# Kernel tuning notes

Measured on AMD Instinct MI355X. Metric: run time of the kernel, lower is better.

The kernel has to match this reference:

```python
import jax, jax.numpy as jnp
from jax import lax
import numpy as np

NINF = -1e10  # matches torch's -10000000000.0 masked fill


def setup_inputs() -> dict:
    B, T, Z, S1, X = 512, 1024, 8, 5, 2  # S1 = 2**stim_types + 1
    key = jax.random.key(0)
    k1, k2, k3, k4, k5, k6 = jax.random.split(key, 6)
    s = jax.random.randint(k1, (B, T), 0, S1)
    x = jax.random.randint(k2, (B, T), 0, X)
    mask = (jax.random.uniform(k3, (B, T)) > 0.1).astype(jnp.float32)
    # probability-simplex parameters (the torch model stores normalized pi/P/K)
    pi = jax.nn.softmax(jax.random.normal(k4, (Z,)))
    P = jax.nn.softmax(jax.random.normal(k5, (Z, X)), axis=-1)
    K = jax.nn.softmax(jax.random.normal(k6, (S1, Z, Z)), axis=-2)  # columns sum to 1 over 'to'
    return {"s": s, "x": x, "mask": mask, "pi": pi, "P": P, "K": K}


def reference(s, x, mask, pi, P, K):
    B, T = x.shape
    Z = pi.shape[0]
    logpi = jnp.log(pi)
    logP = jnp.log(P)            # (Z, X)
    logKb = jnp.log(K)[s]        # (B, T, Z, Z), [to, from]
    logPx = logP.T[x]            # (B, T, Z)

    # ---- forward pass: masked alpha recurrence ----
    def fstep(prev, inp):
        lK, lP, m = inp          # (B,Z,Z), (B,Z), (B,)
        new = (jax.nn.logsumexp(prev[:, None, :] + lK, axis=-1) + lP) * m[:, None] \
              + prev * (1.0 - m)[:, None]
        return new, new

    prev0 = jnp.broadcast_to(logpi[None, :], (B, Z))
    _, alphas = lax.scan(fstep, prev0,
                         (logKb.transpose(1, 0, 2, 3), logPx.transpose(1, 0, 2), mask.T))
    log_alpha = alphas.transpose(1, 0, 2)                 # (B, T, Z)
    loglik = jax.nn.logsumexp(log_alpha[:, -1, :], axis=-1)  # (B,)

    # ---- backward pass: masked beta recurrence (carries masked P/K 'next') ----
    def bstep(carry, inp):
        bn, lPn, lKn = carry
        lK_t, lP_t, m0, m1 = inp  # mask[t], mask[t+1]
        bt = jax.nn.logsumexp(lPn[:, :, None] + lKn + bn[:, :, None], axis=1) * m1[:, None] \
             + bn * (1.0 - m1)[:, None]
        lPn2 = lP_t * m0[:, None] + lPn * (1.0 - m0)[:, None]
        lKn2 = lK_t * m0[:, None, None] + lKn * (1.0 - m0)[:, None, None]
        return (bt, lPn2, lKn2), bt

    carry0 = (jnp.zeros((B, Z)), logPx[:, -1], logKb[:, -1])
    xs = (logKb[:, :-1].transpose(1, 0, 2, 3), logPx[:, :-1].transpose(1, 0, 2),
          mask[:, :-1].T, mask[:, 1:].T)
    _, betas = lax.scan(bstep, carry0, xs, reverse=True)
    log_beta = jnp.concatenate([betas.transpose(1, 0, 2), jnp.zeros((B, 1, Z))], axis=1)

    # ---- posteriors ----
    log_beta = log_beta - loglik[:, None, None]
    log_gamma = log_alpha + log_beta
    log_gamma = log_gamma - jax.nn.logsumexp(log_gamma, axis=-1, keepdims=True)
    log_xi = logKb[:, :-1] + log_alpha[:, :-1, :, None] + log_beta[:, 1:, None, :] \
             + logPx[:, 1:][:, :, None, :]
    log_xi = log_xi - jax.nn.logsumexp(log_xi.reshape(B, T - 1, -1), axis=-1)[:, :, None, None]
    log_gamma = jnp.where((mask == 0)[:, :, None], NINF, log_gamma)
    log_xi = jnp.where((mask[:, 1:] == 0)[:, :, None, None], NINF, log_xi)
    return log_gamma, log_xi, log_alpha, log_beta, loglik
```

## Files before the change

### kernel.cpp

```cpp
#include <hip/hip_runtime.h>

#define BB 512
#define TT 1024
#define GG 32
#define LL 32
#define NINF -10000000000.0f
#define SROW 65
#define NXROWS (BB * (TT - 1))
#define SCRATCH_ROW0 484375

template<int CTRL>
__device__ __forceinline__ float dppf(float x) {
    return __builtin_bit_cast(float, __builtin_amdgcn_update_dpp(
        0, __builtin_bit_cast(int, x), CTRL, 0xF, 0xF, true));
}
__device__ __forceinline__ float gsum8(float x) {
    x += dppf<0xB1>(x); x += dppf<0x4E>(x); x += dppf<0x141>(x); return x;
}
__device__ __forceinline__ float gmax8(float x) {
    x = fmaxf(x, dppf<0xB1>(x)); x = fmaxf(x, dppf<0x4E>(x)); x = fmaxf(x, dppf<0x141>(x)); return x;
}

#define GATHER8(A0, A1, A2, A3, A4, A5, A6, A7)      \
    const float A1 = dppf<0xB1>(A0);                 \
    const float A2 = dppf<0x4E>(A0);                 \
    const float A7 = dppf<0x141>(A0);                \
    const float A3 = dppf<0x4E>(A1);                 \
    const float A6 = dppf<0xB1>(A7);                 \
    const float A5 = dppf<0x4E>(A7);                 \
    const float A4 = dppf<0x4E>(A6);

#define FMASUM(ACC, K0, K1, A0,A1,A2,A3,A4,A5,A6,A7) \
    float ACC;                                       \
    {   float accA = K0.x * A0;                      \
        accA = fmaf(K0.y, A1, accA);                 \
        accA = fmaf(K0.z, A2, accA);                 \
        accA = fmaf(K0.w, A3, accA);                 \
        float accB = K1.x * A4;                      \
        accB = fmaf(K1.y, A5, accB);                 \
        accB = fmaf(K1.z, A6, accB);                 \
        ACC = accA + accB; }

__global__ __launch_bounds__(256) void segmat_kernel(
    const int* __restrict__ s, const int* __restrict__ x, const float* __restrict__ mask,
    const float* __restrict__ P, const float* __restrict__ K,
    float* __restrict__ FM, float* __restrict__ BM)
{
    __shared__ float kTab[5 * 68];
    __shared__ int   ctrlA[4][LL];
    const int tid = threadIdx.x;
    const int wv = tid >> 6, l = tid & 63;
    const int lo = l & 7, hi = l >> 3;
    const bool isF = blockIdx.x < 4096;
    const int task = (isF ? blockIdx.x : blockIdx.x - 4096) * 4 + wv;
    const int seq = task >> 5, seg = task & 31;
    const int sb = seq * TT;
    const int t0 = seg * LL;

    for (int e = tid; e < 340; e += 256) {
        const int ss = e / 68, idx = e - ss * 68;
        float v = 0.0f;
        if (idx < 64) {
            const int row = idx >> 3, r = idx & 7;
            v = isF ? K[ss*64 + row*8 + (row ^ r)]
                    : K[ss*64 + (row ^ r)*8 + row];
        }
        kTab[e] = v;
    }
    if (l < LL) {
        const int tt = t0 + l;
        ctrlA[wv][l] = s[sb+tt] | (x[sb+tt] << 3) | ((mask[sb+tt] != 0.0f) ? 16 : 0);
    }
    __syncthreads();

    const float pL0 = P[lo*2+0], pL1 = P[lo*2+1];
    const float* kbase = kTab + lo*8;
    float av = (lo == hi) ? 1.0f : 0.0f;
    float c = 0.0f;

    if (isF) {
#pragma unroll 4
        for (int u = 0; u < LL; ++u) {
            const int cw = __builtin_amdgcn_readfirstlane(ctrlA[wv][u]);
            if (cw & 16) {
                const float* kp = kbase + (cw & 7) * 68;
                const float4 k0 = *(const float4*)kp;
                const float4 k1 = *(const float4*)(kp + 4);
                const float a0 = av;
                GATHER8(a0, a1, a2, a3, a4, a5, a6, a7)
                FMASUM(acc, k0, k1, a0,a1,a2,a3,a4,a5,a6,a7)
                av = acc * ((cw & 8) ? pL1 : pL0);
            }
            if ((u & 3) == 3) {
                const float ms = gmax8(av);
                av *= __builtin_amdgcn_rcpf(ms);
                c += __logf(ms);
            }
        }
        FM[task*64 + l] = __logf(av) + c;
    } else {
        const int t1 = t0 + LL;
        int sxc = 0;
        for (int tt = t1; tt < TT; ++tt) {
            if (mask[sb + tt] != 0.0f) { sxc = s[sb+tt] | (x[sb+tt] << 3); break; }
        }
        int m1 = (t1 < TT && mask[sb + t1] != 0.0f) ? 16 : 0;
        sxc = __builtin_amdgcn_readfirstlane(sxc);
        m1  = __builtin_amdgcn_readfirstlane(m1);
#pragma unroll 4
        for (int u = LL - 1; u >= 0; --u) {
            const int cw = __builtin_amdgcn_readfirstlane(ctrlA[wv][u]);
            if (m1) {
                const float* kp = kbase + (sxc & 7) * 68;
                const float4 k0 = *(const float4*)kp;
                const float4 k1 = *(const float4*)(kp + 4);
                const float u0 = av * ((sxc & 8) ? pL1 : pL0);
                GATHER8(u0, u1, u2, u3, u4, u5, u6, u7)
                FMASUM(acc, k0, k1, u0,u1,u2,u3,u4,u5,u6,u7)
                av = acc;
            }
            sxc = (cw & 16) ? (cw & 15) : sxc;
            m1 = cw & 16;
            if ((u & 3) == 0) {
                const float ms = gmax8(av);
                av *= __builtin_amdgcn_rcpf(ms);
                c += __logf(ms);
            }
        }
        BM[task*64 + l] = __logf(av) + c;
    }
}

__global__ __launch_bounds__(256) void compose_kernel(
    const float* __restrict__ pi, const float* __restrict__ FM, const float* __restrict__ BM,
    float* __restrict__ SV, float* __restrict__ WV, float* __restrict__ loglik)
{
    const int tid = threadIdx.x;
    const int grp = blockIdx.x * 32 + (tid >> 3);
    const int i = tid & 7;
    if (grp < BB) {
        const int seq = grp;
        float v = __logf(pi[i]);
        for (int g = 0; g < GG; ++g) {
            SV[(seq*GG + g)*8 + i] = v;
            const float* M = FM + (size_t)(seq*GG + g) * 64;
            const float a0 = v;
            GATHER8(a0, a1, a2, a3, a4, a5, a6, a7)
            const float q0 = M[(i^0)*8 + i] + a0;
            const float q1 = M[(i^1)*8 + i] + a1;
            const float q2 = M[(i^2)*8 + i] + a2;
            const float q3 = M[(i^3)*8 + i] + a3;
            const float q4 = M[(i^4)*8 + i] + a4;
            const float q5 = M[(i^5)*8 + i] + a5;
            const float q6 = M[(i^6)*8 + i] + a6;
            const float q7 = M[(i^7)*8 + i] + a7;
            float m = fmaxf(q0, q1); m = fmaxf(m, q2); m = fmaxf(m, q3);
            m = fmaxf(m, q4); m = fmaxf(m, q5); m = fmaxf(m, q6); m = fmaxf(m, q7);
            float sum = __expf(q0-m) + __expf(q1-m) + __expf(q2-m) + __expf(q3-m)
                      + __expf(q4-m) + __expf(q5-m) + __expf(q6-m) + __expf(q7-m);
            v = m + __logf(sum);
        }
        const float gm = gmax8(v);
        const float ge = gsum8(__expf(v - gm));
        if (i == 0) loglik[seq] = gm + __logf(ge);
    } else {
        const int seq = grp - BB;
        float v = 0.0f;
        for (int g = GG - 1; g >= 0; --g) {
            WV[(seq*GG + g)*8 + i] = v;
            const float* M = BM + (size_t)(seq*GG + g) * 64;
            const float a0 = v;
            GATHER8(a0, a1, a2, a3, a4, a5, a6, a7)
            const float q0 = M[(i^0)*8 + i] + a0;
            const float q1 = M[(i^1)*8 + i] + a1;
            const float q2 = M[(i^2)*8 + i] + a2;
            const float q3 = M[(i^3)*8 + i] + a3;
            const float q4 = M[(i^4)*8 + i] + a4;
            const float q5 = M[(i^5)*8 + i] + a5;
            const float q6 = M[(i^6)*8 + i] + a6;
            const float q7 = M[(i^7)*8 + i] + a7;
            float m = fmaxf(q0, q1); m = fmaxf(m, q2); m = fmaxf(m, q3);
            m = fmaxf(m, q4); m = fmaxf(m, q5); m = fmaxf(m, q6); m = fmaxf(m, q7);
            float sum = __expf(q0-m) + __expf(q1-m) + __expf(q2-m) + __expf(q3-m)
                      + __expf(q4-m) + __expf(q5-m) + __expf(q6-m) + __expf(q7-m);
            v = m + __logf(sum);
        }
    }
}

__global__ __launch_bounds__(256) void fused_kernel(
    const int* __restrict__ s, const int* __restrict__ x, const float* __restrict__ mask,
    const float* __restrict__ P, const float* __restrict__ K,
    const float* __restrict__ SV, const float* __restrict__ WV,
    const float* __restrict__ loglik,
    float* __restrict__ alpha, float* __restrict__ beta,
    float* __restrict__ gamma, float* __restrict__ xi, int skipRow0)
{
    __shared__ float aLs[2 * 32 * SROW];
    __shared__ float bLs[2 * 33 * SROW];
    __shared__ int   ctrlL[2 * 33 * 8];
    __shared__ float kX[340], kTt[340];
    __shared__ float lK[320], lP[16];

    const int tid = threadIdx.x;
    const int wv = tid >> 6, l = tid & 63;
    const int lo = l & 7, g = l >> 3;
    const int sgp = blockIdx.x >> 4;
    const int pairIdx = blockIdx.x & 15;
    const int bfirst = sgp * 8;
    const int segi = wv >> 1;
    const bool isFwd = (wv & 1) == 0;
    const int seg = pairIdx * 2 + segi;
    const int t0 = seg * LL;
    const int seq = bfirst + g;
    const int sb = seq * TT;

    for (int e = tid; e < 340; e += 256) {
        const int ss = e / 68, idx = e - ss * 68;
        float vX = 0.0f, vT = 0.0f;
        if (idx < 64) {
            const int row = idx >> 3, r = idx & 7;
            vX = K[ss*64 + row*8 + (row ^ r)];
            vT = K[ss*64 + (row ^ r)*8 + row];
        }
        kX[e] = vX; kTt[e] = vT;
    }
    for (int e = tid; e < 320; e += 256) lK[e] = __logf(K[e]);
    if (tid < 16) lP[tid] = __logf(P[tid]);
    for (int e = tid; e < 528; e += 256) {
        const int si = e / 264, rem = e - si * 264;
        const int u = rem >> 3, gg = rem & 7;
        const int t = (pairIdx*2 + si)*LL + u;
        int cv = 0;
        if (t < TT) {
            const int a = (bfirst + gg)*TT + t;
            cv = s[a] | (x[a] << 3) | ((mask[a] != 0.0f) ? 16 : 0);
        }
        ctrlL[(si*33 + u)*8 + gg] = cv;
    }
    __syncthreads();

    const float pL0 = P[lo*2+0], pL1 = P[lo*2+1];

    if (isFwd) {
        const float sv0 = SV[(seq*GG + seg)*8 + lo];
        const float mx = gmax8(sv0);
        float av = __expf(sv0 - mx);
        float c = mx;
        size_t aoff = (size_t)(sb + t0)*8 + lo;
#pragma unroll 4
        for (int u = 0; u < LL; ++u) {
            const int cw = ctrlL[(segi*33 + u)*8 + g];
            const float* kp = kX + (cw & 7)*68 + lo*8;
            const float4 k0 = *(const float4*)kp;
            const float4 k1 = *(const float4*)(kp + 4);
            const float a0 = av;
            GATHER8(a0, a1, a2, a3, a4, a5, a6, a7)
            FMASUM(acc, k0, k1, a0,a1,a2,a3,a4,a5,a6,a7)
            const float nv = acc * ((cw & 8) ? pL1 : pL0);
            av = (cw & 16) ? nv : av;
            if ((u & 3) == 3) {
                const float ms = gmax8(av);
                av *= __builtin_amdgcn_rcpf(ms);
                c += __logf(ms);
            }
            const float la = __logf(av) + c;
            aLs[(segi*32 + u)*SROW + g*8 + lo] = la;
            __builtin_nontemporal_store(la, &alpha[aoff]);
            aoff += 8;
        }
    } else {
        const float w0 = WV[(seq*GG + seg)*8 + lo];
        const float llv = loglik[seq];
        const float mx = gmax8(w0);
        float bv = __expf(w0 - mx);
        float c = mx - llv;
        bLs[(segi*33 + 32)*SROW + g*8 + lo] = w0 - llv;
        const int t1 = t0 + LL;
        int m1 = ctrlL[(segi*33 + 32)*8 + g] & 16;
        int sxc = 0;
        {
            int tt = t1;
            int found = (t1 >= TT) ? 1 : 0;
            while (!__all(found)) {
                if (!found && tt < TT) {
                    if (mask[sb + tt] != 0.0f) { sxc = s[sb+tt] | (x[sb+tt] << 3); found = 1; }
                }
                if (tt >= TT - 1) found = 1;
                ++tt;
            }
        }
        size_t boff = (size_t)(sb + t1 - 1)*8 + lo;
#pragma unroll 4
        for (int u = LL - 1; u >= 0; --u) {
            const int cw = ctrlL[(segi*33 + u)*8 + g];
            const float* kp = kTt + (sxc & 7)*68 + lo*8;
            const float4 k0 = *(const float4*)kp;
            const float4 k1 = *(const float4*)(kp + 4);
            const float u0 = bv * ((sxc & 8) ? pL1 : pL0);
            GATHER8(u0, u1, u2, u3, u4, u5, u6, u7)
            FMASUM(acc, k0, k1, u0,u1,u2,u3,u4,u5,u6,u7)
            bv = m1 ? acc : bv;
            if ((u & 3) == 0) {
                const float ms = gmax8(bv);
                bv *= __builtin_amdgcn_rcpf(ms);
                c += __logf(ms);
            }
            const float lb = __logf(bv) + c;
            bLs[(segi*33 + u)*SROW + g*8 + lo] = lb;
            __builtin_nontemporal_store(lb, &beta[boff]);
            boff -= 8;
            sxc = (cw & 16) ? (cw & 15) : sxc;
            m1 = cw & 16;
        }
    }
    __syncthreads();

    for (int it = 0; it < 16; ++it) {
        const int r = wv*128 + it*8 + (l >> 3);
        const int si = r >> 8, rr = r & 255, sq = rr >> 5, u = rr & 31;
        const int t = (pairIdx*2 + si)*LL + u;
        const int z = l & 7;
        const int cw = ctrlL[(si*33 + u)*8 + sq];
        const float gv = (cw & 16)
            ? (aLs[(si*32 + u)*SROW + sq*8 + z] + bLs[(si*33 + u)*SROW + sq*8 + z])
            : NINF;
        __builtin_nontemporal_store(gv, &gamma[((size_t)(bfirst+sq)*TT + t)*8 + z]);
    }
    for (int it = 0; it < 128; ++it) {
        const int r = wv*128 + it;
        const int si = r >> 8, rr = r & 255, sq = rr >> 5, u = rr & 31;
        const int t = (pairIdx*2 + si)*LL + u;
        if (t >= TT - 1) continue;
        const int rowLin = (bfirst + sq)*(TT - 1) + t;
        if (rowLin >= skipRow0) continue;
        const int cw  = ctrlL[(si*33 + u)*8 + sq];
        const int cw1 = ctrlL[(si*33 + u + 1)*8 + sq];
        float xo = NINF;
        if (cw1 & 16) {
            const float aHi = aLs[(si*32 + u)*SROW + sq*8 + (l >> 3)];
            const float bN  = bLs[(si*33 + u + 1)*SROW + sq*8 + (l & 7)];
            xo = lK[(cw & 7)*64 + l] + aHi + bN + lP[(l & 7)*2 + ((cw1 >> 3) & 1)];
        }
        __builtin_nontemporal_store(xo, &xi[(size_t)rowLin*64 + l]);
    }
}

__global__ __launch_bounds__(256) void xi_fixup_kernel(
    const int* __restrict__ s, const int* __restrict__ x, const float* __restrict__ mask,
    const float* __restrict__ P, const float* __restrict__ K,
    const float* __restrict__ alpha, const float* __restrict__ beta,
    float* __restrict__ xi)
{
    __shared__ float lK[320], lP[16];
    const int tid = threadIdx.x;
    for (int e = tid; e < 320; e += 256) lK[e] = __logf(K[e]);
    if (tid < 16) lP[tid] = __logf(P[tid]);
    __syncthreads();

    const int wv = tid >> 6, l = tid & 63;
    const int row = SCRATCH_ROW0 + blockIdx.x * 4 + wv;
    if (row >= NXROWS) return;
    const int b = row / (TT - 1);
    const int t = row - b * (TT - 1);
    const long bt = (long)b * TT + t;
    float xo = NINF;
    if (mask[bt + 1] != 0.0f) {
        const int sv = s[bt];
        const int xv = x[bt + 1];
        const float aHi = alpha[bt*8 + (l >> 3)];
        const float bN  = beta[(bt + 1)*8 + (l & 7)];
        xo = lK[sv*64 + l] + aHi + bN + lP[(l & 7)*2 + xv];
    }
    xi[(size_t)row*64 + l] = xo;
}

extern "C" void kernel_launch(void* const* d_in, const int* in_sizes, int n_in,
                              void* d_out, int out_size, void* d_ws, size_t ws_size,
                              hipStream_t stream) {
    const int*   s    = (const int*)d_in[0];
    const int*   x    = (const int*)d_in[1];
    const float* mask = (const float*)d_in[2];
    const float* pi   = (const float*)d_in[3];
    const float* P    = (const float*)d_in[4];
    const float* K    = (const float*)d_in[5];

    float* out    = (float*)d_out;
    float* gamma  = out;
    float* xi     = gamma + (size_t)BB * TT * 8;
    float* alpha  = xi + (size_t)BB * (TT - 1) * 64;
    float* beta   = alpha + (size_t)BB * TT * 8;
    float* loglik = beta + (size_t)BB * TT * 8;

    const size_t scratchFloats = (size_t)2*BB*GG*64 + (size_t)2*BB*GG*8;
    const bool useWs = ws_size >= scratchFloats * sizeof(float);
    float* FMs = useWs ? (float*)d_ws : xi + (size_t)31000000;
    float* BMs = FMs + (size_t)BB * GG * 64;
    float* SVs = BMs + (size_t)BB * GG * 64;
    float* WVs = SVs + (size_t)BB * GG * 8;
    const int skipRow0 = useWs ? 0x7FFFFFFF : SCRATCH_ROW0;

    segmat_kernel<<<8192, 256, 0, stream>>>(s, x, mask, P, K, FMs, BMs);
    compose_kernel<<<32, 256, 0, stream>>>(pi, FMs, BMs, SVs, WVs, loglik);
    fused_kernel<<<1024, 256, 0, stream>>>(s, x, mask, P, K, SVs, WVs, loglik,
                                           alpha, beta, gamma, xi, skipRow0);
    if (!useWs) {
        const int tailRows = NXROWS - SCRATCH_ROW0;
        xi_fixup_kernel<<<(tailRows + 3) / 4, 256, 0, stream>>>(
            s, x, mask, P, K, alpha, beta, xi);
    }
}
```

Baseline: 125.2 us.

## Vectorize output stores as float4 and move alpha/beta writes out of recurrence loops

```diff
diff --git a/kernel.cpp b/kernel.cpp
--- a/kernel.cpp
+++ b/kernel.cpp
@@ -5,9 +5,11 @@
 #define GG 32
 #define LL 32
 #define NINF -10000000000.0f
-#define SROW 65
+#define SROW 68
 #define NXROWS (BB * (TT - 1))
 #define SCRATCH_ROW0 484375
+
+typedef float fvec4 __attribute__((ext_vector_type(4)));
 
 template<int CTRL>
 __device__ __forceinline__ float dppf(float x) {
@@ -200,7 +202,8 @@
     __shared__ float bLs[2 * 33 * SROW];
     __shared__ int   ctrlL[2 * 33 * 8];
     __shared__ float kX[340], kTt[340];
-    __shared__ float lK[320], lP[16];
+    __shared__ float lK[320];
+    __shared__ float lP0[8], lP1[8];
 
     const int tid = threadIdx.x;
     const int wv = tid >> 6, l = tid & 63;
@@ -226,7 +229,7 @@
         kX[e] = vX; kTt[e] = vT;
     }
     for (int e = tid; e < 320; e += 256) lK[e] = __logf(K[e]);
-    if (tid < 16) lP[tid] = __logf(P[tid]);
+    if (tid < 8) { lP0[tid] = __logf(P[tid*2]); lP1[tid] = __logf(P[tid*2+1]); }
     for (int e = tid; e < 528; e += 256) {
         const int si = e / 264, rem = e - si * 264;
         const int u = rem >> 3, gg = rem & 7;
@@ -247,7 +250,6 @@
         const float mx = gmax8(sv0);
         float av = __expf(sv0 - mx);
         float c = mx;
-        size_t aoff = (size_t)(sb + t0)*8 + lo;
 #pragma unroll 4
         for (int u = 0; u < LL; ++u) {
             const int cw = ctrlL[(segi*33 + u)*8 + g];
@@ -264,10 +266,7 @@
                 av *= __builtin_amdgcn_rcpf(ms);
                 c += __logf(ms);
             }
-            const float la = __logf(av) + c;
-            aLs[(segi*32 + u)*SROW + g*8 + lo] = la;
-            __builtin_nontemporal_store(la, &alpha[aoff]);
-            aoff += 8;
+            aLs[(segi*32 + u)*SROW + g*8 + lo] = __logf(av) + c;
         }
     } else {
         const float w0 = WV[(seq*GG + seg)*8 + lo];
@@ -290,7 +289,6 @@
                 ++tt;
             }
         }
-        size_t boff = (size_t)(sb + t1 - 1)*8 + lo;
 #pragma unroll 4
         for (int u = LL - 1; u >= 0; --u) {
             const int cw = ctrlL[(segi*33 + u)*8 + g];
@@ -306,43 +304,59 @@
                 bv *= __builtin_amdgcn_rcpf(ms);
                 c += __logf(ms);
             }
-            const float lb = __logf(bv) + c;
-            bLs[(segi*33 + u)*SROW + g*8 + lo] = lb;
-            __builtin_nontemporal_store(lb, &beta[boff]);
-            boff -= 8;
+            bLs[(segi*33 + u)*SROW + g*8 + lo] = __logf(bv) + c;
             sxc = (cw & 16) ? (cw & 15) : sxc;
             m1 = cw & 16;
         }
     }
     __syncthreads();
 
-    for (int it = 0; it < 16; ++it) {
-        const int r = wv*128 + it*8 + (l >> 3);
-        const int si = r >> 8, rr = r & 255, sq = rr >> 5, u = rr & 31;
-        const int t = (pairIdx*2 + si)*LL + u;
-        const int z = l & 7;
-        const int cw = ctrlL[(si*33 + u)*8 + sq];
-        const float gv = (cw & 16)
-            ? (aLs[(si*32 + u)*SROW + sq*8 + z] + bLs[(si*33 + u)*SROW + sq*8 + z])
-            : NINF;
-        __builtin_nontemporal_store(gv, &gamma[((size_t)(bfirst+sq)*TT + t)*8 + z]);
-    }
-    for (int it = 0; it < 128; ++it) {
-        const int r = wv*128 + it;
-        const int si = r >> 8, rr = r & 255, sq = rr >> 5, u = rr & 31;
-        const int t = (pairIdx*2 + si)*LL + u;
+    const int t0base = pairIdx * 64;
+    for (int it = 0; it < 4; ++it) {
+        const int f4 = it*256 + tid;
+        const int sq = f4 >> 7;
+        const int rem = f4 & 127;
+        const int tl = rem >> 1, z4 = (rem & 1) * 4;
+        const int si = tl >> 5, u = tl & 31;
+        const size_t gbase = ((size_t)(bfirst+sq)*TT + t0base + tl)*8 + z4;
+        const float4 av4 = *(const float4*)&aLs[(si*32+u)*SROW + sq*8 + z4];
+        const float4 bv4 = *(const float4*)&bLs[(si*33+u)*SROW + sq*8 + z4];
+        __builtin_nontemporal_store(__builtin_bit_cast(fvec4, av4), (fvec4*)&alpha[gbase]);
+        __builtin_nontemporal_store(__builtin_bit_cast(fvec4, bv4), (fvec4*)&beta[gbase]);
+        float4 gv;
+        if (ctrlL[(si*33+u)*8 + sq] & 16) {
+            gv.x = av4.x + bv4.x; gv.y = av4.y + bv4.y;
+            gv.z = av4.z + bv4.z; gv.w = av4.w + bv4.w;
+        } else { gv.x = NINF; gv.y = NINF; gv.z = NINF; gv.w = NINF; }
+        __builtin_nontemporal_store(__builtin_bit_cast(fvec4, gv), (fvec4*)&gamma[gbase]);
+    }
+    for (int it = 0; it < 32; ++it) {
+        const int f4 = it*256 + tid;
+        const int r = f4 >> 4, ll2 = f4 & 15;
+        const int sq = r >> 6, tl = r & 63;
+        const int t = t0base + tl;
         if (t >= TT - 1) continue;
         const int rowLin = (bfirst + sq)*(TT - 1) + t;
         if (rowLin >= skipRow0) continue;
+        const int si = tl >> 5, u = tl & 31;
         const int cw  = ctrlL[(si*33 + u)*8 + sq];
         const int cw1 = ctrlL[(si*33 + u + 1)*8 + sq];
-        float xo = NINF;
+        float4 o;
         if (cw1 & 16) {
-            const float aHi = aLs[(si*32 + u)*SROW + sq*8 + (l >> 3)];
-            const float bN  = bLs[(si*33 + u + 1)*SROW + sq*8 + (l & 7)];
-            xo = lK[(cw & 7)*64 + l] + aHi + bN + lP[(l & 7)*2 + ((cw1 >> 3) & 1)];
-        }
-        __builtin_nontemporal_store(xo, &xi[(size_t)rowLin*64 + l]);
+            const int i = ll2 >> 1, bj = (ll2 & 1)*4;
+            const float aHi = aLs[(si*32 + u)*SROW + sq*8 + i];
+            const float4 bN = *(const float4*)&bLs[(si*33 + u + 1)*SROW + sq*8 + bj];
+            const float4 kv = *(const float4*)&lK[(cw & 7)*64 + ll2*4];
+            const float4 p0 = *(const float4*)&lP0[bj];
+            const float4 p1 = *(const float4*)&lP1[bj];
+            const int xv = (cw1 >> 3) & 1;
+            o.x = kv.x + aHi + bN.x + (xv ? p1.x : p0.x);
+            o.y = kv.y + aHi + bN.y + (xv ? p1.y : p0.y);
+            o.z = kv.z + aHi + bN.z + (xv ? p1.z : p0.z);
+            o.w = kv.w + aHi + bN.w + (xv ? p1.w : p0.w);
+        } else { o.x = NINF; o.y = NINF; o.z = NINF; o.w = NINF; }
+        __builtin_nontemporal_store(__builtin_bit_cast(fvec4, o),
+                                    (fvec4*)&xi[(size_t)rowLin*64 + ll2*4]);
     }
 }
 
```

After: 110.1 us. 12.0% less time.
